# Kernel tuning notes

Hardware: AMD Instinct MI355X
Metric: run time of the kernel (lower is better)

The kernel has to match this reference:

```python
import jax, jax.numpy as jnp
import numpy as np

B, S, D = 4, 4096, 1024
DFF = 4 * D
ACTIVE = 1024  # ceil(S * 0.25)


def setup_inputs() -> dict:
    key = jax.random.key(0)
    ks = jax.random.split(key, 4)
    x = jax.random.normal(ks[0], (B, S, D), dtype=jnp.float32)
    rw = jax.random.normal(ks[1], (D,), dtype=jnp.float32) * 0.02
    rb = jnp.zeros((1,), dtype=jnp.float32)
    w1 = jax.random.normal(ks[2], (D, DFF), dtype=jnp.float32) * 0.02
    b1 = jnp.zeros((DFF,), dtype=jnp.float32)
    w2 = jax.random.normal(ks[3], (DFF, D), dtype=jnp.float32) * 0.02
    b2 = jnp.zeros((D,), dtype=jnp.float32)
    return {"x": x, "rw": rw, "rb": rb, "w1": w1, "b1": b1,
            "w2": w2, "b2": b2, "active_tokens": ACTIVE}


def reference(x, rw, rb, w1, b1, w2, b2, active_tokens):
    b, s, d = x.shape
    # router: Linear(n_embd, 1) -> [B, S] scores
    scores = jnp.einsum('bsd,d->bs', x, rw) + rb[0]
    # top-k tokens per batch row
    _, idx = jax.lax.top_k(scores, active_tokens)          # [B, K] int32
    sel = jnp.take_along_axis(x, idx[..., None], axis=1)   # [B, K, D]
    # dense MLP on selected tokens (exact GELU as in torch nn.GELU)
    h = jax.nn.gelu(jnp.einsum('bkd,df->bkf', sel, w1) + b1, approximate=False)
    out = jnp.einsum('bkf,fd->bkd', h, w2) + b2            # [B, K, D]
    # sigmoid gate from router scores of selected tokens
    gates = jax.nn.sigmoid(jnp.take_along_axis(scores, idx, axis=1))  # [B, K]
    out = out * gates[..., None]
    # scatter back into zeros at selected positions
    flat_idx = (idx + jnp.arange(b, dtype=idx.dtype)[:, None] * s).reshape(-1)
    flat_out = jnp.zeros((b * s, d), dtype=out.dtype)
    flat_out = flat_out.at[flat_idx].set(out.reshape(-1, d))
    return flat_out.reshape(b, s, d)
```

## Files before the change

### kernel.cpp

```cpp
#include <hip/hip_runtime.h>
#include <hip/hip_bf16.h>
#include <cstdint>
#include <cstddef>

#define Bz 4
#define Sz 4096
#define Dz 1024
#define DFFz 4096
#define KACT 1024

typedef __bf16 bf16;
typedef __attribute__((ext_vector_type(8))) __bf16 bf16x8;
typedef __attribute__((ext_vector_type(4))) __bf16 bf16x4;
typedef __attribute__((ext_vector_type(4))) float f32x4;

__device__ __forceinline__ void async16(const void* g, void* l) {
  __builtin_amdgcn_global_load_lds(
      (const __attribute__((address_space(1))) void*)g,
      (__attribute__((address_space(3))) void*)l, 16, 0, 0);
}

__global__ __launch_bounds__(256) void prep_k(const float* __restrict__ x,
                                              const float* __restrict__ rw,
                                              const float* __restrict__ rb,
                                              float* __restrict__ scores,
                                              float4* __restrict__ out4,
                                              const float* __restrict__ w1,
                                              bf16* __restrict__ w1T,
                                              const float* __restrict__ w2,
                                              bf16* __restrict__ w2T) {
  __shared__ float t[32][33];
  const int bid = blockIdx.x;
  const int tid = threadIdx.x;
  if (bid < 4096) {
    int row = bid * 4 + (tid >> 6);
    int lane = tid & 63;
    const float4* xr = (const float4*)(x + (size_t)row * Dz);
    const float4* wr = (const float4*)rw;
    float acc = 0.f;
#pragma unroll
    for (int i = 0; i < 4; ++i) {
      float4 a = xr[lane + i * 64];
      float4 w = wr[lane + i * 64];
      acc += a.x * w.x + a.y * w.y + a.z * w.z + a.w * w.w;
    }
#pragma unroll
    for (int d = 32; d; d >>= 1) acc += __shfl_down(acc, d, 64);
    if (lane == 0) scores[row] = acc + rb[0];
    float4* o = out4 + (size_t)bid * 4 * (Dz / 4);
    const float4 z = make_float4(0.f, 0.f, 0.f, 0.f);
#pragma unroll
    for (int i = 0; i < 4; ++i) o[tid + i * 256] = z;
  } else {
    const float* in; bf16* outp; int R, C, bx, by;
    if (bid < 8192) {
      in = w1; outp = w1T; R = Dz; C = DFFz;
      bx = (bid - 4096) & 127; by = (bid - 4096) >> 7;
    } else {
      in = w2; outp = w2T; R = DFFz; C = Dz;
      bx = (bid - 8192) & 31; by = (bid - 8192) >> 5;
    }
    int c0 = bx * 32, r0 = by * 32;
    int tx = tid & 31, ty = tid >> 5;
#pragma unroll
    for (int i = 0; i < 32; i += 8) t[ty + i][tx] = in[(size_t)(r0 + ty + i) * C + c0 + tx];
    __syncthreads();
#pragma unroll
    for (int i = 0; i < 32; i += 8)
      outp[(size_t)(c0 + ty + i) * R + r0 + tx] = (bf16)t[tx][ty + i];
  }
}

__global__ __launch_bounds__(256) void select_gather_k(
    const float* __restrict__ x, const float* __restrict__ scores,
    int* __restrict__ sel_idx, float* __restrict__ gates, bf16* __restrict__ Xsel) {
  int b = blockIdx.x >> 8;
  int s0 = (blockIdx.x & 255) * 16;
  __shared__ float sc[Sz];
  __shared__ int red[16][4];
  __shared__ int rk[16];
  const int tid = threadIdx.x;
  const int wave = tid >> 6, lane = tid & 63;
  const float* srow = scores + (size_t)b * Sz;
#pragma unroll
  for (int i = 0; i < 4; ++i)
    ((float4*)sc)[tid + i * 256] = ((const float4*)srow)[tid + i * 256];
  __syncthreads();
  float mine[16];
#pragma unroll
  for (int j = 0; j < 16; ++j) mine[j] = sc[s0 + j];
  int cnt[16] = {};
  for (int t = tid; t < Sz; t += 256) {
    float o = sc[t];
#pragma unroll
    for (int j = 0; j < 16; ++j)
      cnt[j] += (o > mine[j]) || (o == mine[j] && t < s0 + j);
  }
#pragma unroll
  for (int j = 0; j < 16; ++j) {
    int c = cnt[j];
#pragma unroll
    for (int d = 32; d; d >>= 1) c += __shfl_down(c, d, 64);
    if (lane == 0) red[j][wave] = c;
  }
  __syncthreads();
  if (tid < 16) {
    int rank = red[tid][0] + red[tid][1] + red[tid][2] + red[tid][3];
    rk[tid] = rank;
    if (rank < KACT) {
      int m = b * KACT + rank;
      sel_idx[m] = s0 + tid;
      gates[m] = 1.f / (1.f + expf(-sc[s0 + tid]));
    }
  }
  __syncthreads();
#pragma unroll
  for (int j = 0; j < 16; ++j) {
    int rank = rk[j];
    if (rank >= KACT) continue;
    int m = b * KACT + rank;
    float4 v = ((const float4*)(x + ((size_t)b * Sz + s0 + j) * Dz))[tid];
    bf16x4 o = {(bf16)v.x, (bf16)v.y, (bf16)v.z, (bf16)v.w};
    ((bf16x4*)(Xsel + (size_t)m * Dz))[tid] = o;
  }
}


__global__ __launch_bounds__(256) void gemm1_k(const bf16* __restrict__ A,
                                               const bf16* __restrict__ Bt,
                                               const float* __restrict__ bias,
                                               bf16* __restrict__ H) {
  __shared__ __align__(16) bf16 As[2][128 * 32];
  __shared__ __align__(16) bf16 Bs[2][128 * 32];
  constexpr int K = Dz;
  constexpr int NITER = Dz / 32;
  const int tid = threadIdx.x;
  const int wave = tid >> 6, lane = tid & 63;
  const int quad = lane >> 4, l16 = lane & 15;
  const int orig = blockIdx.y * 32 + blockIdx.x;
  const int swz = ((orig & 7) << 7) | (orig >> 3);
  const int m0 = (swz >> 5) * 128, n0 = (swz & 31) * 128;
  const int wm = (wave >> 1) * 64, wn = (wave & 1) * 64;
  const bf16* Ag = A + (size_t)(m0 + (tid >> 2)) * K + (tid & 3) * 8;
  const bf16* Bg = Bt + (size_t)(n0 + (tid >> 2)) * K + (tid & 3) * 8;
  f32x4 acc[4][4] = {};
  async16(Ag, &As[0][tid * 8]);
  async16(Ag + (size_t)64 * K, &As[0][2048 + tid * 8]);
  async16(Bg, &Bs[0][tid * 8]);
  async16(Bg + (size_t)64 * K, &Bs[0][2048 + tid * 8]);
  __syncthreads();
  for (int t = 0; t < NITER; ++t) {
    const int cur = t & 1;
    if (t + 1 < NITER) {
      const int k0 = (t + 1) * 32;
      async16(Ag + k0, &As[cur ^ 1][tid * 8]);
      async16(Ag + (size_t)64 * K + k0, &As[cur ^ 1][2048 + tid * 8]);
      async16(Bg + k0, &Bs[cur ^ 1][tid * 8]);
      async16(Bg + (size_t)64 * K + k0, &Bs[cur ^ 1][2048 + tid * 8]);
    }
    bf16x8 af[4], bfr[4];
#pragma unroll
    for (int i = 0; i < 4; ++i) {
      af[i] = *(const bf16x8*)&As[cur][(wm + i * 16 + l16) * 32 + quad * 8];
      bfr[i] = *(const bf16x8*)&Bs[cur][(wn + i * 16 + l16) * 32 + quad * 8];
    }
    __builtin_amdgcn_s_setprio(1);
#pragma unroll
    for (int mi = 0; mi < 4; ++mi)
#pragma unroll
      for (int ni = 0; ni < 4; ++ni)
        acc[mi][ni] = __builtin_amdgcn_mfma_f32_16x16x32_bf16(af[mi], bfr[ni], acc[mi][ni], 0, 0, 0);
    __builtin_amdgcn_s_setprio(0);
    __syncthreads();
  }
#pragma unroll
  for (int mi = 0; mi < 4; ++mi) {
    int mbase = m0 + wm + mi * 16 + quad * 4;
#pragma unroll
    for (int ni = 0; ni < 4; ++ni) {
      int n = n0 + wn + ni * 16 + l16;
      float bn = bias[n];
#pragma unroll
      for (int r = 0; r < 4; ++r) {
        float z = acc[mi][ni][r] + bn;
        float g = 0.5f * z * (1.f + erff(z * 0.70710678118654752f));
        H[(size_t)(mbase + r) * DFFz + n] = (bf16)g;
      }
    }
  }
}

__global__ __launch_bounds__(256) void gemm2_k(const bf16* __restrict__ A,
                                               const bf16* __restrict__ Bt,
                                               const float* __restrict__ b2,
                                               const int* __restrict__ sel_idx,
                                               const float* __restrict__ gates,
                                               float* __restrict__ out) {
  __shared__ __align__(16) bf16 As[2][128 * 32];
  __shared__ __align__(16) bf16 Bs[2][64 * 32];
  constexpr int K = DFFz;
  constexpr int NITER = DFFz / 32;
  const int tid = threadIdx.x;
  const int wave = tid >> 6, lane = tid & 63;
  const int quad = lane >> 4, l16 = lane & 15;
  const int orig = blockIdx.y * 16 + blockIdx.x;
  const int swz = ((orig & 7) << 6) | (orig >> 3);
  const int m0 = (swz >> 4) * 128, n0 = (swz & 15) * 64;
  const int wm = (wave >> 1) * 64, wn = (wave & 1) * 32;
  const bf16* Ag = A + (size_t)(m0 + (tid >> 2)) * K + (tid & 3) * 8;
  const bf16* Bg = Bt + (size_t)(n0 + (tid >> 2)) * K + (tid & 3) * 8;
  f32x4 acc[4][2] = {};
  async16(Ag, &As[0][tid * 8]);
  async16(Ag + (size_t)64 * K, &As[0][2048 + tid * 8]);
  async16(Bg, &Bs[0][tid * 8]);
  __syncthreads();
  for (int t = 0; t < NITER; ++t) {
    const int cur = t & 1;
    if (t + 1 < NITER) {
      const int k0 = (t + 1) * 32;
      async16(Ag + k0, &As[cur ^ 1][tid * 8]);
      async16(Ag + (size_t)64 * K + k0, &As[cur ^ 1][2048 + tid * 8]);
      async16(Bg + k0, &Bs[cur ^ 1][tid * 8]);
    }
    bf16x8 af[4], bfr[2];
#pragma unroll
    for (int i = 0; i < 4; ++i)
      af[i] = *(const bf16x8*)&As[cur][(wm + i * 16 + l16) * 32 + quad * 8];
#pragma unroll
    for (int i = 0; i < 2; ++i)
      bfr[i] = *(const bf16x8*)&Bs[cur][(wn + i * 16 + l16) * 32 + quad * 8];
    __builtin_amdgcn_s_setprio(1);
#pragma unroll
    for (int mi = 0; mi < 4; ++mi)
#pragma unroll
      for (int ni = 0; ni < 2; ++ni)
        acc[mi][ni] = __builtin_amdgcn_mfma_f32_16x16x32_bf16(af[mi], bfr[ni], acc[mi][ni], 0, 0, 0);
    __builtin_amdgcn_s_setprio(0);
    __syncthreads();
  }
#pragma unroll
  for (int mi = 0; mi < 4; ++mi) {
#pragma unroll
    for (int r = 0; r < 4; ++r) {
      int m = m0 + wm + mi * 16 + quad * 4 + r;
      int b = m >> 10;
      int s = sel_idx[m];
      float g = gates[m];
      float* orow = out + ((size_t)b * Sz + s) * Dz;
#pragma unroll
      for (int ni = 0; ni < 2; ++ni) {
        int n = n0 + wn + ni * 16 + l16;
        orow[n] = (acc[mi][ni][r] + b2[n]) * g;
      }
    }
  }
}

extern "C" void kernel_launch(void* const* d_in, const int* in_sizes, int n_in,
                              void* d_out, int out_size, void* d_ws, size_t ws_size,
                              hipStream_t stream) {
  (void)in_sizes; (void)n_in; (void)out_size; (void)ws_size;
  const float* x  = (const float*)d_in[0];
  const float* rw = (const float*)d_in[1];
  const float* rb = (const float*)d_in[2];
  const float* w1 = (const float*)d_in[3];
  const float* b1 = (const float*)d_in[4];
  const float* w2 = (const float*)d_in[5];
  const float* b2 = (const float*)d_in[6];
  float* out = (float*)d_out;

  char* ws = (char*)d_ws;
  float* scores = (float*)ws;  ws += (size_t)Bz * Sz * 4;
  int*   sel_idx = (int*)ws;   ws += (size_t)Bz * KACT * 4;
  float* gates = (float*)ws;   ws += (size_t)Bz * KACT * 4;
  bf16*  w2T = (bf16*)ws;      ws += (size_t)Dz * DFFz * 2;
  bf16*  H = (bf16*)ws;        ws += (size_t)Bz * KACT * DFFz * 2;
  bf16*  w1T = (bf16*)ws;      ws += (size_t)DFFz * Dz * 2;
  bf16*  Xsel = (bf16*)ws;     ws += (size_t)Bz * KACT * Dz * 2;

  prep_k<<<3 * 4096, 256, 0, stream>>>(x, rw, rb, scores, (float4*)out, w1, w1T, w2, w2T);
  select_gather_k<<<Bz * (Sz / 16), 256, 0, stream>>>(x, scores, sel_idx, gates, Xsel);
  gemm1_k<<<dim3(DFFz / 128, (Bz * KACT) / 128), 256, 0, stream>>>(Xsel, w1T, b1, H);
  gemm2_k<<<dim3(Dz / 64, (Bz * KACT) / 128), 256, 0, stream>>>(H, w2T, b2, sel_idx, gates, out);
}
```

Before: 325.4 us.

## Use triple-buffered swizzled LDS pipelines and larger tiles in both GEMMs

Both GEMMs move from a double-buffered LDS pipeline to a three-stage one. Each iteration now waits with an explicit vmcnt barrier instead of a full __syncthreads, so loads run two tiles ahead. LDS addresses are XOR-swizzled to reduce bank conflicts. GEMM1 grows to 256x256 tiles with 512 threads, and GEMM2 grows to 128x128 tiles, giving more reuse per load. The costs are higher register pressure, fewer workgroups (256 per GEMM), and risk in the hand-written waitcnt logic.

Result: slower. 345.1 us (+6.1%).

```diff
diff --git a/kernel.cpp b/kernel.cpp
--- a/kernel.cpp
+++ b/kernel.cpp
@@ -126,56 +126,83 @@
 }
 
 
-__global__ __launch_bounds__(256) void gemm1_k(const bf16* __restrict__ A,
-                                               const bf16* __restrict__ Bt,
-                                               const float* __restrict__ bias,
-                                               bf16* __restrict__ H) {
-  __shared__ __align__(16) bf16 As[2][128 * 32];
-  __shared__ __align__(16) bf16 Bs[2][128 * 32];
+#define BAR_VM4 asm volatile("s_waitcnt vmcnt(4) lgkmcnt(0)\n\ts_barrier" ::: "memory")
+#define BAR_VM0 asm volatile("s_waitcnt vmcnt(0) lgkmcnt(0)\n\ts_barrier" ::: "memory")
+
+__global__ __launch_bounds__(512, 2) void gemm1_k(const bf16* __restrict__ A,
+                                                  const bf16* __restrict__ Bt,
+                                                  const float* __restrict__ bias,
+                                                  bf16* __restrict__ H) {
+  __shared__ __align__(16) bf16 SA[3][8192];
+  __shared__ __align__(16) bf16 SB[3][8192];
   constexpr int K = Dz;
-  constexpr int NITER = Dz / 32;
+  constexpr int NITER = K / 32;
   const int tid = threadIdx.x;
   const int wave = tid >> 6, lane = tid & 63;
   const int quad = lane >> 4, l16 = lane & 15;
-  const int orig = blockIdx.y * 32 + blockIdx.x;
-  const int swz = ((orig & 7) << 7) | (orig >> 3);
-  const int m0 = (swz >> 5) * 128, n0 = (swz & 31) * 128;
-  const int wm = (wave >> 1) * 64, wn = (wave & 1) * 64;
-  const bf16* Ag = A + (size_t)(m0 + (tid >> 2)) * K + (tid & 3) * 8;
-  const bf16* Bg = Bt + (size_t)(n0 + (tid >> 2)) * K + (tid & 3) * 8;
-  f32x4 acc[4][4] = {};
-  async16(Ag, &As[0][tid * 8]);
-  async16(Ag + (size_t)64 * K, &As[0][2048 + tid * 8]);
-  async16(Bg, &Bs[0][tid * 8]);
-  async16(Bg + (size_t)64 * K, &Bs[0][2048 + tid * 8]);
-  __syncthreads();
+  const int orig = blockIdx.y * 16 + blockIdx.x;
+  const int wgid = (orig & 7) * 32 + (orig >> 3);
+  const int m0 = (wgid >> 4) * 256, n0 = (wgid & 15) * 256;
+  const int wm = (wave >> 2) * 128, wn = (wave & 3) * 64;
+  const int Ld0 = tid * 16, Ld1 = 8192 + tid * 16;
+  const int q0 = Ld0 ^ (((Ld0 >> 7) & 3) << 4);
+  const int q1 = Ld1 ^ (((Ld1 >> 7) & 3) << 4);
+  const char* pa0 = (const char*)A + ((size_t)(m0 + (q0 >> 6)) * K) * 2 + (q0 & 63);
+  const char* pa1 = (const char*)A + ((size_t)(m0 + (q1 >> 6)) * K) * 2 + (q1 & 63);
+  const char* pb0 = (const char*)Bt + ((size_t)(n0 + (q0 >> 6)) * K) * 2 + (q0 & 63);
+  const char* pb1 = (const char*)Bt + ((size_t)(n0 + (q1 >> 6)) * K) * 2 + (q1 & 63);
+  int aoff[8], boff[4];
+#pragma unroll
+  for (int i = 0; i < 8; ++i) {
+    int r = wm + i * 16 + l16;
+    int off = r * 64 + quad * 16;
+    aoff[i] = off ^ (((r >> 1) & 3) << 4);
+  }
+#pragma unroll
+  for (int i = 0; i < 4; ++i) {
+    int r = wn + i * 16 + l16;
+    int off = r * 64 + quad * 16;
+    boff[i] = off ^ (((r >> 1) & 3) << 4);
+  }
+#define STAGE1(sel, t)                                                      \
+  {                                                                         \
+    char* dA = (char*)&SA[sel][0];                                          \
+    char* dB = (char*)&SB[sel][0];                                          \
+    size_t ko = (size_t)(t) * 64;                                           \
+    async16(pa0 + ko, dA + Ld0);                                            \
+    async16(pa1 + ko, dA + Ld1);                                            \
+    async16(pb0 + ko, dB + Ld0);                                            \
+    async16(pb1 + ko, dB + Ld1);                                            \
+  }
+  f32x4 acc[8][4] = {};
+  STAGE1(0, 0)
+  STAGE1(1, 1)
+  BAR_VM4;
   for (int t = 0; t < NITER; ++t) {
-    const int cur = t & 1;
-    if (t + 1 < NITER) {
-      const int k0 = (t + 1) * 32;
-      async16(Ag + k0, &As[cur ^ 1][tid * 8]);
-      async16(Ag + (size_t)64 * K + k0, &As[cur ^ 1][2048 + tid * 8]);
-      async16(Bg + k0, &Bs[cur ^ 1][tid * 8]);
-      async16(Bg + (size_t)64 * K + k0, &Bs[cur ^ 1][2048 + tid * 8]);
-    }
-    bf16x8 af[4], bfr[4];
-#pragma unroll
-    for (int i = 0; i < 4; ++i) {
-      af[i] = *(const bf16x8*)&As[cur][(wm + i * 16 + l16) * 32 + quad * 8];
-      bfr[i] = *(const bf16x8*)&Bs[cur][(wn + i * 16 + l16) * 32 + quad * 8];
-    }
+    const int sel = t % 3;
+    const bool more = (t + 2 < NITER);
+    if (more) { const int s2 = (t + 2) % 3; STAGE1(s2, t + 2) }
+    const char* a = (const char*)&SA[sel][0];
+    const char* b = (const char*)&SB[sel][0];
+    bf16x8 af[8], bfr[4];
+#pragma unroll
+    for (int i = 0; i < 8; ++i) af[i] = *(const bf16x8*)(a + aoff[i]);
+#pragma unroll
+    for (int i = 0; i < 4; ++i) bfr[i] = *(const bf16x8*)(b + boff[i]);
     __builtin_amdgcn_s_setprio(1);
 #pragma unroll
-    for (int mi = 0; mi < 4; ++mi)
+    for (int mi = 0; mi < 8; ++mi)
 #pragma unroll
       for (int ni = 0; ni < 4; ++ni)
         acc[mi][ni] = __builtin_amdgcn_mfma_f32_16x16x32_bf16(af[mi], bfr[ni], acc[mi][ni], 0, 0, 0);
     __builtin_amdgcn_s_setprio(0);
-    __syncthreads();
-  }
-#pragma unroll
-  for (int mi = 0; mi < 4; ++mi) {
-    int mbase = m0 + wm + mi * 16 + quad * 4;
+    if (more) { BAR_VM4; }
+    else if (t + 2 == NITER) { BAR_VM0; }
+  }
+#undef STAGE1
+#pragma unroll
+  for (int mi = 0; mi < 8; ++mi) {
+    int mb = m0 + wm + mi * 16 + quad * 4;
 #pragma unroll
     for (int ni = 0; ni < 4; ++ni) {
       int n = n0 + wn + ni * 16 + l16;
@@ -184,7 +211,7 @@
       for (int r = 0; r < 4; ++r) {
         float z = acc[mi][ni][r] + bn;
         float g = 0.5f * z * (1.f + erff(z * 0.70710678118654752f));
-        H[(size_t)(mbase + r) * DFFz + n] = (bf16)g;
+        H[(size_t)(mb + r) * DFFz + n] = (bf16)g;
       }
     }
   }
@@ -196,48 +223,70 @@
                                                const int* __restrict__ sel_idx,
                                                const float* __restrict__ gates,
                                                float* __restrict__ out) {
-  __shared__ __align__(16) bf16 As[2][128 * 32];
-  __shared__ __align__(16) bf16 Bs[2][64 * 32];
+  __shared__ __align__(16) bf16 SA[3][4096];
+  __shared__ __align__(16) bf16 SB[3][4096];
   constexpr int K = DFFz;
-  constexpr int NITER = DFFz / 32;
+  constexpr int NITER = K / 32;
   const int tid = threadIdx.x;
   const int wave = tid >> 6, lane = tid & 63;
   const int quad = lane >> 4, l16 = lane & 15;
-  const int orig = blockIdx.y * 16 + blockIdx.x;
-  const int swz = ((orig & 7) << 6) | (orig >> 3);
-  const int m0 = (swz >> 4) * 128, n0 = (swz & 15) * 64;
-  const int wm = (wave >> 1) * 64, wn = (wave & 1) * 32;
-  const bf16* Ag = A + (size_t)(m0 + (tid >> 2)) * K + (tid & 3) * 8;
-  const bf16* Bg = Bt + (size_t)(n0 + (tid >> 2)) * K + (tid & 3) * 8;
-  f32x4 acc[4][2] = {};
-  async16(Ag, &As[0][tid * 8]);
-  async16(Ag + (size_t)64 * K, &As[0][2048 + tid * 8]);
-  async16(Bg, &Bs[0][tid * 8]);
-  __syncthreads();
+  const int orig = blockIdx.y * 8 + blockIdx.x;
+  const int wgid = (orig & 7) * 32 + (orig >> 3);
+  const int m0 = (wgid >> 3) * 128, n0 = (wgid & 7) * 128;
+  const int wm = (wave >> 1) * 64, wn = (wave & 1) * 64;
+  const int Ld0 = tid * 16, Ld1 = 4096 + tid * 16;
+  const int q0 = Ld0 ^ (((Ld0 >> 7) & 3) << 4);
+  const int q1 = Ld1 ^ (((Ld1 >> 7) & 3) << 4);
+  const char* pa0 = (const char*)A + ((size_t)(m0 + (q0 >> 6)) * K) * 2 + (q0 & 63);
+  const char* pa1 = (const char*)A + ((size_t)(m0 + (q1 >> 6)) * K) * 2 + (q1 & 63);
+  const char* pb0 = (const char*)Bt + ((size_t)(n0 + (q0 >> 6)) * K) * 2 + (q0 & 63);
+  const char* pb1 = (const char*)Bt + ((size_t)(n0 + (q1 >> 6)) * K) * 2 + (q1 & 63);
+  int aoff[4], boff[4];
+#pragma unroll
+  for (int i = 0; i < 4; ++i) {
+    int ra = wm + i * 16 + l16;
+    int oa = ra * 64 + quad * 16;
+    aoff[i] = oa ^ (((ra >> 1) & 3) << 4);
+    int rb = wn + i * 16 + l16;
+    int ob = rb * 64 + quad * 16;
+    boff[i] = ob ^ (((rb >> 1) & 3) << 4);
+  }
+#define STAGE2(sel, t)                                                      \
+  {                                                                         \
+    char* dA = (char*)&SA[sel][0];                                          \
+    char* dB = (char*)&SB[sel][0];                                          \
+    size_t ko = (size_t)(t) * 64;                                           \
+    async16(pa0 + ko, dA + Ld0);                                            \
+    async16(pa1 + ko, dA + Ld1);                                            \
+    async16(pb0 + ko, dB + Ld0);                                            \
+    async16(pb1 + ko, dB + Ld1);                                            \
+  }
+  f32x4 acc[4][4] = {};
+  STAGE2(0, 0)
+  STAGE2(1, 1)
+  BAR_VM4;
   for (int t = 0; t < NITER; ++t) {
-    const int cur = t & 1;
-    if (t + 1 < NITER) {
-      const int k0 = (t + 1) * 32;
-      async16(Ag + k0, &As[cur ^ 1][tid * 8]);
-      async16(Ag + (size_t)64 * K + k0, &As[cur ^ 1][2048 + tid * 8]);
-      async16(Bg + k0, &Bs[cur ^ 1][tid * 8]);
-    }
-    bf16x8 af[4], bfr[2];
-#pragma unroll
-    for (int i = 0; i < 4; ++i)
-      af[i] = *(const bf16x8*)&As[cur][(wm + i * 16 + l16) * 32 + quad * 8];
-#pragma unroll
-    for (int i = 0; i < 2; ++i)
-      bfr[i] = *(const bf16x8*)&Bs[cur][(wn + i * 16 + l16) * 32 + quad * 8];
+    const int sel = t % 3;
+    const bool more = (t + 2 < NITER);
+    if (more) { const int s2 = (t + 2) % 3; STAGE2(s2, t + 2) }
+    const char* a = (const char*)&SA[sel][0];
+    const char* b = (const char*)&SB[sel][0];
+    bf16x8 af[4], bfr[4];
+#pragma unroll
+    for (int i = 0; i < 4; ++i) af[i] = *(const bf16x8*)(a + aoff[i]);
+#pragma unroll
+    for (int i = 0; i < 4; ++i) bfr[i] = *(const bf16x8*)(b + boff[i]);
     __builtin_amdgcn_s_setprio(1);
 #pragma unroll
     for (int mi = 0; mi < 4; ++mi)
 #pragma unroll
-      for (int ni = 0; ni < 2; ++ni)
+      for (int ni = 0; ni < 4; ++ni)
         acc[mi][ni] = __builtin_amdgcn_mfma_f32_16x16x32_bf16(af[mi], bfr[ni], acc[mi][ni], 0, 0, 0);
     __builtin_amdgcn_s_setprio(0);
-    __syncthreads();
-  }
+    if (more) { BAR_VM4; }
+    else if (t + 2 == NITER) { BAR_VM0; }
+  }
+#undef STAGE2
 #pragma unroll
   for (int mi = 0; mi < 4; ++mi) {
 #pragma unroll
@@ -248,7 +297,7 @@
       float g = gates[m];
       float* orow = out + ((size_t)b * Sz + s) * Dz;
 #pragma unroll
-      for (int ni = 0; ni < 2; ++ni) {
+      for (int ni = 0; ni < 4; ++ni) {
         int n = n0 + wn + ni * 16 + l16;
         orow[n] = (acc[mi][ni][r] + b2[n]) * g;
       }
@@ -280,6 +329,6 @@
 
   prep_k<<<3 * 4096, 256, 0, stream>>>(x, rw, rb, scores, (float4*)out, w1, w1T, w2, w2T);
   select_gather_k<<<Bz * (Sz / 16), 256, 0, stream>>>(x, scores, sel_idx, gates, Xsel);
-  gemm1_k<<<dim3(DFFz / 128, (Bz * KACT) / 128), 256, 0, stream>>>(Xsel, w1T, b1, H);
-  gemm2_k<<<dim3(Dz / 64, (Bz * KACT) / 128), 256, 0, stream>>>(H, w2T, b2, sel_idx, gates, out);
-}
+  gemm1_k<<<dim3(16, 16), 512, 0, stream>>>(Xsel, w1T, b1, H);
+  gemm2_k<<<dim3(8, 32), 256, 0, stream>>>(H, w2T, b2, sel_idx, gates, out);
+}
```
